# Kernel tuning notes

Hardware: AMD Instinct MI355X
Metric: run time of the kernel (lower is better)

## Reference

```python
import jax, jax.numpy as jnp
import numpy as np

SIZE = 128
BATCH = 64
STEEPNESS = 10.0


def _odd_even_indices(n):
    """Odd-even transposition sorting network: n layers of disjoint adjacent pairs.
    All layers are padded to k = n//2 pairs with self-pairs (i,i)=(0,0), which are
    exact no-ops under the soft compare-exchange (matches pass-through wires of the
    original network)."""
    k = n // 2
    ia, ib = [], []
    for layer in range(n):
        start = layer % 2
        pa = list(range(start, n - 1, 2))
        pb = [i + 1 for i in pa]
        while len(pa) < k:  # pad with no-op self-pairs
            pa.append(0)
            pb.append(0)
        ia.append(pa)
        ib.append(pb)
    return jnp.asarray(np.array(ia, np.int32)), jnp.asarray(np.array(ib, np.int32))


def setup_inputs() -> dict:
    key = jax.random.key(0)
    return {"vectors": jax.random.normal(key, (BATCH, SIZE), dtype=jnp.float32)}


def _soft_sort(vectors):
    Bsz, n = vectors.shape
    ia, ib = _odd_even_indices(n)  # [n_layers, k] each
    x0 = vectors
    # X[b, i, j] = soft probability mass of input element i at output slot j,
    # i.e. the invariant  x[b] == vectors[b] @ X[b]  holds after every layer.
    X0 = jnp.tile(jnp.eye(n, dtype=vectors.dtype)[None], (Bsz, 1, 1))
    inv_pi = jnp.float32(1.0 / np.pi)

    def step(carry, idx):
        x, X = carry
        a_idx, b_idx = idx
        a = x[:, a_idx]  # [B, k]
        b = x[:, b_idx]  # [B, k]
        # Cauchy CDF relaxation of the comparison (module default distribution)
        alpha = jnp.arctan(STEEPNESS * (b - a)) * inv_pi + 0.5
        x = x.at[:, a_idx].set(alpha * a + (1.0 - alpha) * b)        # soft min
        x = x.at[:, b_idx].set((1.0 - alpha) * a + alpha * b)        # soft max
        A = X[:, :, a_idx]   # [B, n, k] columns feeding the 'a' wires
        Bc = X[:, :, b_idx]  # [B, n, k] columns feeding the 'b' wires
        w = alpha[:, None, :]
        X = X.at[:, :, a_idx].set(w * A + (1.0 - w) * Bc)
        X = X.at[:, :, b_idx].set((1.0 - w) * A + w * Bc)
        return (x, X), None

    (x, X), _ = jax.lax.scan(step, (x0, X0), (ia, ib))
    return x, X


def reference(vectors):
    # Returns (softly sorted values [B, n], relaxed permutation matrix [B, n, n])
    return _soft_sort(vectors)
```

## Files before the change

### kernel.cpp

```cpp
#include <hip/hip_runtime.h>
#include <math.h>

#define SIZE 128
#define BATCH 64
#define STEEP 10.0f
#define G 8
#define NG 8

template<int CTRL>
__device__ __forceinline__ float dpp_mov(float x) {
    return __int_as_float(__builtin_amdgcn_update_dpp(
        __float_as_int(x), __float_as_int(x), CTRL, 0xf, 0xf, false));
}

__device__ __forceinline__ float alpha_from_delta(float delta) {
    const float C0 =  0.31830265f;
    const float C1 = -0.10587730f;
    const float C2 =  0.06160680f;
    const float C3 = -0.03706173f;
    const float C4 =  0.01676007f;
    const float C5 = -0.00373098f;
    float t  = STEEP * delta;
    float at = fabsf(t);
    bool inv = at > 1.0f;
    float z  = inv ? __builtin_amdgcn_rcpf(at) : at;
    float z2 = z * z, z4 = z2 * z2;
    float p0 = fmaf(C1, z2, C0);
    float p1 = fmaf(C3, z2, C2);
    float p2 = fmaf(C5, z2, C4);
    float q  = fmaf(fmaf(p2, z4, p1), z4, p0) * z;
    float r  = inv ? 0.5f - q : q;
    return 0.5f + copysignf(r, t);
}

__global__ __launch_bounds__(576) void soft_sort_fused(
    const float* __restrict__ vec, float* __restrict__ out)
{
    __shared__ float alds[2][2 * G * 64];

    const int tid    = threadIdx.x;
    const int lane   = tid & 63;
    const int wave   = tid >> 6;
    const int batch  = blockIdx.x >> 2;
    const int rowgrp = blockIdx.x & 3;

    if (wave == 8) {
        const int c0 = 2 * lane;
        const float2 xv = *reinterpret_cast<const float2*>(vec + batch * SIZE + c0);
        float xa = xv.x, xb = xv.y;
        const bool hasR = (lane < 63);
        const bool hasL = (lane > 0);

        for (int grp = 0; grp < NG; ++grp) {
            float* buf = &alds[grp & 1][0];
#pragma unroll
            for (int j = 0; j < G; ++j) {
                const float d  = xb - xa;
                const float ae = alpha_from_delta(d);
                buf[(2 * j) * 64 + lane] = ae;
                const float nxa0 = fmaf(-ae, d, xb);
                const float nxb0 = fmaf( ae, d, xa);
                const float xnext = dpp_mov<0x130>(nxa0);
                float ao = alpha_from_delta(xnext - nxb0);
                ao = hasR ? ao : 1.0f;
                buf[(2 * j + 1) * 64 + lane] = ao;
                float aoL = dpp_mov<0x138>(ao);
                aoL = hasL ? aoL : 1.0f;
                const float xprev = dpp_mov<0x138>(nxb0);
                xb = fmaf(ao,  nxb0 - xnext, xnext);
                xa = fmaf(aoL, nxa0 - xprev, xprev);
            }
            __syncthreads();
        }
        if (rowgrp == 0)
            *reinterpret_cast<float2*>(out + batch * SIZE + c0) = make_float2(xa, xb);
    } else {
        const int chunk   = lane & 15;
        const int row_sub = lane >> 4;
        const int row     = rowgrp * 32 + wave * 4 + row_sub;
        const int c8      = chunk * 8;
        const int q4      = chunk * 4;
        const int qm      = (chunk > 0) ? q4 - 1 : 63;

        float v[8];
#pragma unroll
        for (int j = 0; j < 8; ++j) v[j] = (row == c8 + j) ? 1.0f : 0.0f;

        for (int grp = 0; grp < NG; ++grp) {
            __syncthreads();
            const float* buf = &alds[grp & 1][0];
            float4 ae = *reinterpret_cast<const float4*>(buf + q4);
            float4 ao = *reinterpret_cast<const float4*>(buf + 64 + q4);
            float  aL = buf[64 + qm];
#pragma unroll
            for (int j = 0; j < G; ++j) {
                const int nj = (j < G - 1) ? j + 1 : j;
                const float4 ae_n = *reinterpret_cast<const float4*>(buf + (2 * nj) * 64 + q4);
                const float4 ao_n = *reinterpret_cast<const float4*>(buf + (2 * nj + 1) * 64 + q4);
                const float  aL_n = buf[(2 * nj + 1) * 64 + qm];

                float A, B, d;
                A = v[0]; B = v[1]; d = A - B; v[0] = fmaf(ae.x, d, B); v[1] = fmaf(-ae.x, d, A);
                A = v[2]; B = v[3]; d = A - B; v[2] = fmaf(ae.y, d, B); v[3] = fmaf(-ae.y, d, A);
                A = v[4]; B = v[5]; d = A - B; v[4] = fmaf(ae.z, d, B); v[5] = fmaf(-ae.z, d, A);
                A = v[6]; B = v[7]; d = A - B; v[6] = fmaf(ae.w, d, B); v[7] = fmaf(-ae.w, d, A);
                const float nb0 = dpp_mov<0x101>(v[0]);
                const float pb7 = dpp_mov<0x111>(v[7]);
                A = v[1]; B = v[2]; d = A - B; v[1] = fmaf(ao.x, d, B); v[2] = fmaf(-ao.x, d, A);
                A = v[3]; B = v[4]; d = A - B; v[3] = fmaf(ao.y, d, B); v[4] = fmaf(-ao.y, d, A);
                A = v[5]; B = v[6]; d = A - B; v[5] = fmaf(ao.z, d, B); v[6] = fmaf(-ao.z, d, A);
                v[7] = fmaf(ao.w, v[7] - nb0, nb0);
                v[0] = fmaf(aL,   v[0] - pb7, pb7);

                ae = ae_n; ao = ao_n; aL = aL_n;
            }
        }

        float* __restrict__ X = out + BATCH * SIZE + (batch * SIZE + row) * SIZE + c8;
        *reinterpret_cast<float4*>(X)     = make_float4(v[0], v[1], v[2], v[3]);
        *reinterpret_cast<float4*>(X + 4) = make_float4(v[4], v[5], v[6], v[7]);
    }
}

extern "C" void kernel_launch(void* const* d_in, const int* in_sizes, int n_in,
                              void* d_out, int out_size, void* d_ws, size_t ws_size,
                              hipStream_t stream) {
    const float* vec = (const float*)d_in[0];
    float* out = (float*)d_out;
    (void)in_sizes; (void)n_in; (void)d_ws; (void)ws_size; (void)out_size;

    hipLaunchKernelGGL(soft_sort_fused, dim3(BATCH * 4), dim3(576), 0, stream,
                       vec, out);
}
```

Baseline: 69.11 us.

## Process two matrix rows per lane with smaller blocks and more blocks per batch

Each matrix-lane now carries two rows (va/vb) instead of one, so a block has 2 matrix waves plus 1 alpha wave covering 16 rows. The grid doubles to 8 blocks per batch. This raises instruction-level parallelism in the dependent FMA chains and reuses each LDS alpha load across two rows. In exchange, the alpha computation wave is duplicated across more blocks, and the number of waves sharing each alpha producer shrinks.

```diff
diff --git a/kernel.cpp b/kernel.cpp
--- a/kernel.cpp
+++ b/kernel.cpp
@@ -33,7 +33,7 @@
     return 0.5f + copysignf(r, t);
 }
 
-__global__ __launch_bounds__(576) void soft_sort_fused(
+__global__ __launch_bounds__(192) void soft_sort_fused(
     const float* __restrict__ vec, float* __restrict__ out)
 {
     __shared__ float alds[2][2 * G * 64];
@@ -41,10 +41,10 @@
     const int tid    = threadIdx.x;
     const int lane   = tid & 63;
     const int wave   = tid >> 6;
-    const int batch  = blockIdx.x >> 2;
-    const int rowgrp = blockIdx.x & 3;
+    const int batch  = blockIdx.x >> 3;
+    const int rowgrp = blockIdx.x & 7;
 
-    if (wave == 8) {
+    if (wave == 2) {
         const int c0 = 2 * lane;
         const float2 xv = *reinterpret_cast<const float2*>(vec + batch * SIZE + c0);
         float xa = xv.x, xb = xv.y;
@@ -75,16 +75,20 @@
         if (rowgrp == 0)
             *reinterpret_cast<float2*>(out + batch * SIZE + c0) = make_float2(xa, xb);
     } else {
-        const int chunk   = lane & 15;
-        const int row_sub = lane >> 4;
-        const int row     = rowgrp * 32 + wave * 4 + row_sub;
-        const int c8      = chunk * 8;
-        const int q4      = chunk * 4;
-        const int qm      = (chunk > 0) ? q4 - 1 : 63;
+        const int chunk = lane & 15;
+        const int rsub  = lane >> 4;
+        const int row0  = rowgrp * 16 + wave * 8 + rsub * 2;
+        const int row1  = row0 + 1;
+        const int c8    = chunk * 8;
+        const int q4    = chunk * 4;
+        const int qm    = (chunk > 0) ? q4 - 1 : 63;
 
-        float v[8];
+        float va[8], vb[8];
 #pragma unroll
-        for (int j = 0; j < 8; ++j) v[j] = (row == c8 + j) ? 1.0f : 0.0f;
+        for (int j = 0; j < 8; ++j) {
+            va[j] = (row0 == c8 + j) ? 1.0f : 0.0f;
+            vb[j] = (row1 == c8 + j) ? 1.0f : 0.0f;
+        }
 
         for (int grp = 0; grp < NG; ++grp) {
             __syncthreads();
@@ -100,25 +104,39 @@
                 const float  aL_n = buf[(2 * nj + 1) * 64 + qm];
 
                 float A, B, d;
-                A = v[0]; B = v[1]; d = A - B; v[0] = fmaf(ae.x, d, B); v[1] = fmaf(-ae.x, d, A);
-                A = v[2]; B = v[3]; d = A - B; v[2] = fmaf(ae.y, d, B); v[3] = fmaf(-ae.y, d, A);
-                A = v[4]; B = v[5]; d = A - B; v[4] = fmaf(ae.z, d, B); v[5] = fmaf(-ae.z, d, A);
-                A = v[6]; B = v[7]; d = A - B; v[6] = fmaf(ae.w, d, B); v[7] = fmaf(-ae.w, d, A);
-                const float nb0 = dpp_mov<0x101>(v[0]);
-                const float pb7 = dpp_mov<0x111>(v[7]);
-                A = v[1]; B = v[2]; d = A - B; v[1] = fmaf(ao.x, d, B); v[2] = fmaf(-ao.x, d, A);
-                A = v[3]; B = v[4]; d = A - B; v[3] = fmaf(ao.y, d, B); v[4] = fmaf(-ao.y, d, A);
-                A = v[5]; B = v[6]; d = A - B; v[5] = fmaf(ao.z, d, B); v[6] = fmaf(-ao.z, d, A);
-                v[7] = fmaf(ao.w, v[7] - nb0, nb0);
-                v[0] = fmaf(aL,   v[0] - pb7, pb7);
+                A = va[0]; B = va[1]; d = A - B; va[0] = fmaf(ae.x, d, B); va[1] = fmaf(-ae.x, d, A);
+                A = va[2]; B = va[3]; d = A - B; va[2] = fmaf(ae.y, d, B); va[3] = fmaf(-ae.y, d, A);
+                A = va[4]; B = va[5]; d = A - B; va[4] = fmaf(ae.z, d, B); va[5] = fmaf(-ae.z, d, A);
+                A = va[6]; B = va[7]; d = A - B; va[6] = fmaf(ae.w, d, B); va[7] = fmaf(-ae.w, d, A);
+                A = vb[0]; B = vb[1]; d = A - B; vb[0] = fmaf(ae.x, d, B); vb[1] = fmaf(-ae.x, d, A);
+                A = vb[2]; B = vb[3]; d = A - B; vb[2] = fmaf(ae.y, d, B); vb[3] = fmaf(-ae.y, d, A);
+                A = vb[4]; B = vb[5]; d = A - B; vb[4] = fmaf(ae.z, d, B); vb[5] = fmaf(-ae.z, d, A);
+                A = vb[6]; B = vb[7]; d = A - B; vb[6] = fmaf(ae.w, d, B); vb[7] = fmaf(-ae.w, d, A);
+                const float nb0a = dpp_mov<0x101>(va[0]);
+                const float pb7a = dpp_mov<0x111>(va[7]);
+                const float nb0b = dpp_mov<0x101>(vb[0]);
+                const float pb7b = dpp_mov<0x111>(vb[7]);
+                A = va[1]; B = va[2]; d = A - B; va[1] = fmaf(ao.x, d, B); va[2] = fmaf(-ao.x, d, A);
+                A = va[3]; B = va[4]; d = A - B; va[3] = fmaf(ao.y, d, B); va[4] = fmaf(-ao.y, d, A);
+                A = va[5]; B = va[6]; d = A - B; va[5] = fmaf(ao.z, d, B); va[6] = fmaf(-ao.z, d, A);
+                A = vb[1]; B = vb[2]; d = A - B; vb[1] = fmaf(ao.x, d, B); vb[2] = fmaf(-ao.x, d, A);
+                A = vb[3]; B = vb[4]; d = A - B; vb[3] = fmaf(ao.y, d, B); vb[4] = fmaf(-ao.y, d, A);
+                A = vb[5]; B = vb[6]; d = A - B; vb[5] = fmaf(ao.z, d, B); vb[6] = fmaf(-ao.z, d, A);
+                va[7] = fmaf(ao.w, va[7] - nb0a, nb0a);
+                va[0] = fmaf(aL,   va[0] - pb7a, pb7a);
+                vb[7] = fmaf(ao.w, vb[7] - nb0b, nb0b);
+                vb[0] = fmaf(aL,   vb[0] - pb7b, pb7b);
 
                 ae = ae_n; ao = ao_n; aL = aL_n;
             }
         }
 
-        float* __restrict__ X = out + BATCH * SIZE + (batch * SIZE + row) * SIZE + c8;
-        *reinterpret_cast<float4*>(X)     = make_float4(v[0], v[1], v[2], v[3]);
-        *reinterpret_cast<float4*>(X + 4) = make_float4(v[4], v[5], v[6], v[7]);
+        float* __restrict__ X0 = out + BATCH * SIZE + (batch * SIZE + row0) * SIZE + c8;
+        float* __restrict__ X1 = out + BATCH * SIZE + (batch * SIZE + row1) * SIZE + c8;
+        *reinterpret_cast<float4*>(X0)     = make_float4(va[0], va[1], va[2], va[3]);
+        *reinterpret_cast<float4*>(X0 + 4) = make_float4(va[4], va[5], va[6], va[7]);
+        *reinterpret_cast<float4*>(X1)     = make_float4(vb[0], vb[1], vb[2], vb[3]);
+        *reinterpret_cast<float4*>(X1 + 4) = make_float4(vb[4], vb[5], vb[6], vb[7]);
     }
 }
 
@@ -129,6 +147,6 @@
     float* out = (float*)d_out;
     (void)in_sizes; (void)n_in; (void)d_ws; (void)ws_size; (void)out_size;
 
-    hipLaunchKernelGGL(soft_sort_fused, dim3(BATCH * 4), dim3(576), 0, stream,
+    hipLaunchKernelGGL(soft_sort_fused, dim3(BATCH * 8), dim3(192), 0, stream,
                        vec, out);
 }
```

Result: slower. 72.68 us (+5.2%).
